# Performance work log

Hardware: AMD Instinct MI355X
Metric: run time of the kernel (lower is better)

Reference implementation:

```python
import jax, jax.numpy as jnp
import numpy as np

N, E = 50000, 800000
IN_F, C, H, OUT_F = 128, 32, 4, 4
HC = H * C
EPS = 1e-5


def gatv2(x, src, dst, ea, Wl, Wr, We, att, bias, concat):
    # x: [N, in], ea: [E, 1], Wl/Wr: [in, H*C], We: [1, H*C], att: [h, C]
    h, c = att.shape
    xl = (x @ Wl).reshape(-1, h, c)          # [N, h, c]
    xr = (x @ Wr).reshape(-1, h, c)          # [N, h, c]
    m = xl[src] + xr[dst] + (ea @ We).reshape(-1, h, c)   # [E, h, c]
    e = jnp.einsum('ehc,hc->eh', jax.nn.leaky_relu(m, 0.2), att)  # [E, h]
    emax = jax.ops.segment_max(e, dst, num_segments=N)
    e = jnp.exp(e - emax[dst])
    denom = jax.ops.segment_sum(e, dst, num_segments=N)
    alpha = e / (denom[dst] + 1e-16)         # [E, h]
    out = jax.ops.segment_sum(alpha[:, :, None] * xl[src], dst, num_segments=N)  # [N, h, c]
    out = out.reshape(N, h * c) if concat else out.mean(axis=1)
    return out + bias


def bn_eval(x, g, b, m, v):
    return (x - m) * jax.lax.rsqrt(v + EPS) * g + b


def setup_inputs() -> dict:
    key = jax.random.key(0)
    ks = iter(jax.random.split(key, 40))
    nrm = lambda shape, s=0.2: jax.random.normal(next(ks), shape, jnp.float32) * s
    d = {}
    d['x'] = jax.random.normal(next(ks), (N, IN_F), jnp.float32)
    d['edge_index'] = jax.random.randint(next(ks), (2, E), 0, N, jnp.int32)
    d['edge_attr'] = jax.random.normal(next(ks), (E, 1), jnp.float32)
    # layer 1
    d['l1_Wl'] = nrm((IN_F, HC)); d['l1_Wr'] = nrm((IN_F, HC))
    d['l1_We'] = nrm((1, HC)); d['l1_att'] = nrm((H, C)); d['l1_b'] = nrm((HC,))
    # layers 2-9 stacked
    d['mid_Wl'] = nrm((8, HC, HC)); d['mid_Wr'] = nrm((8, HC, HC))
    d['mid_We'] = nrm((8, 1, HC)); d['mid_att'] = nrm((8, H, C)); d['mid_b'] = nrm((8, HC))
    # layer 10: heads=1, concat=False
    d['l10_Wl'] = nrm((HC, C)); d['l10_Wr'] = nrm((HC, C))
    d['l10_We'] = nrm((1, C)); d['l10_att'] = nrm((1, C)); d['l10_b'] = nrm((C,))
    # batchnorms (eval mode): bn1-9 stacked, bn10 separate
    d['bn_g'] = jax.random.uniform(next(ks), (9, HC), jnp.float32, 0.5, 1.5)
    d['bn_b'] = nrm((9, HC)); d['bn_m'] = nrm((9, HC))
    d['bn_v'] = jax.random.uniform(next(ks), (9, HC), jnp.float32, 0.5, 1.5)
    d['bn10_g'] = jax.random.uniform(next(ks), (C,), jnp.float32, 0.5, 1.5)
    d['bn10_b'] = nrm((C,)); d['bn10_m'] = nrm((C,))
    d['bn10_v'] = jax.random.uniform(next(ks), (C,), jnp.float32, 0.5, 1.5)
    d['lin_W'] = nrm((C, OUT_F)); d['lin_b'] = nrm((OUT_F,))
    return d


def reference(x, edge_index, edge_attr,
              l1_Wl, l1_Wr, l1_We, l1_att, l1_b,
              mid_Wl, mid_Wr, mid_We, mid_att, mid_b,
              l10_Wl, l10_Wr, l10_We, l10_att, l10_b,
              bn_g, bn_b, bn_m, bn_v,
              bn10_g, bn10_b, bn10_m, bn10_v,
              lin_W, lin_b):
    src, dst = edge_index[0], edge_index[1]
    h = jax.nn.relu(gatv2(x, src, dst, edge_attr, l1_Wl, l1_Wr, l1_We, l1_att, l1_b, True))
    h = bn_eval(h, bn_g[0], bn_b[0], bn_m[0], bn_v[0])
    for i in range(8):  # layers 2-9
        h = jax.nn.relu(gatv2(h, src, dst, edge_attr, mid_Wl[i], mid_Wr[i], mid_We[i], mid_att[i], mid_b[i], True))
        h = bn_eval(h, bn_g[i + 1], bn_b[i + 1], bn_m[i + 1], bn_v[i + 1])
    h = jax.nn.relu(gatv2(h, src, dst, edge_attr, l10_Wl, l10_Wr, l10_We, l10_att, l10_b, False))
    h = bn_eval(h, bn10_g, bn10_b, bn10_m, bn10_v)
    return h @ lin_W + lin_b
```

## Files before the change

kernel.cpp:

```cpp
#include <hip/hip_runtime.h>
#include <math.h>

#define NN 50000
#define EE 800000
#define EPS 1e-5f
#define SCAN_CH 196

#define NEG_BIG (-1e30f)
#define RESCALE_THR 4.0f

#define LO_SCALE 2048.0f
#define LO_INV   (1.0f/2048.0f)

typedef unsigned short u16;
typedef _Float16 f16x8 __attribute__((ext_vector_type(8)));
typedef float f32x4 __attribute__((ext_vector_type(4)));

__device__ __forceinline__ u16 f2h(float f) {
    _Float16 h = (_Float16)f;
    return __builtin_bit_cast(u16, h);
}
__device__ __forceinline__ float h2f(u16 u) {
    return (float)__builtin_bit_cast(_Float16, u);
}

__global__ void hist_kernel(const int* __restrict__ dst, int* cnt) {
    int e = blockIdx.x * blockDim.x + threadIdx.x;
    if (e < EE) atomicAdd(&cnt[dst[e]], 1);
}

__global__ void scan_part(const int* __restrict__ cnt, int* __restrict__ part) {
    __shared__ int red[256];
    int b = blockIdx.x, t = threadIdx.x;
    int i = b * SCAN_CH + t;
    int v = (t < SCAN_CH && i < NN) ? cnt[i] : 0;
    red[t] = v;
    __syncthreads();
#pragma unroll
    for (int s = 128; s; s >>= 1) {
        if (t < s) red[t] += red[t + s];
        __syncthreads();
    }
    if (t == 0) part[b] = red[0];
}

__global__ void scan_block(int* part) {
    __shared__ int buf[2][256];
    int t = threadIdx.x;
    int v = part[t];
    int p = 0;
    buf[0][t] = v;
    __syncthreads();
#pragma unroll
    for (int off = 1; off < 256; off <<= 1) {
        buf[p ^ 1][t] = buf[p][t] + ((t >= off) ? buf[p][t - off] : 0);
        __syncthreads();
        p ^= 1;
    }
    part[t] = buf[p][t] - v;
}

__global__ void scan_final(int* __restrict__ cntcur, const int* __restrict__ part,
                           int* __restrict__ row_start) {
    __shared__ int buf[2][256];
    int b = blockIdx.x, t = threadIdx.x;
    int i = b * SCAN_CH + t;
    int v = (t < SCAN_CH && i < NN) ? cntcur[i] : 0;
    int p = 0;
    buf[0][t] = v;
    __syncthreads();
#pragma unroll
    for (int off = 1; off < 256; off <<= 1) {
        buf[p ^ 1][t] = buf[p][t] + ((t >= off) ? buf[p][t - off] : 0);
        __syncthreads();
        p ^= 1;
    }
    if (t < SCAN_CH && i < NN) {
        int pos = part[b] + buf[p][t] - v;
        row_start[i] = pos;
        cntcur[i] = pos;
    }
    if (b == 0 && t == 0) row_start[NN] = EE;
}

__global__ void scatter_kernel(const int* __restrict__ ei, const float* __restrict__ ea,
                               int* cursor, int2* __restrict__ edge_pack) {
    int e = blockIdx.x * blockDim.x + threadIdx.x;
    if (e < EE) {
        int d = ei[EE + e];
        int pos = atomicAdd(&cursor[d], 1);
        edge_pack[pos] = make_int2(ei[e], __float_as_int(ea[e]));
    }
}

__global__ void split_f32(const float* __restrict__ in, u16* __restrict__ hi,
                          u16* __restrict__ lo, int n4) {
    int i = blockIdx.x * blockDim.x + threadIdx.x;
    if (i >= n4) return;
    float4 v = ((const float4*)in)[i];
    ushort4 h, l;
    h.x = f2h(v.x); l.x = f2h((v.x - h2f(h.x)) * LO_SCALE);
    h.y = f2h(v.y); l.y = f2h((v.y - h2f(h.y)) * LO_SCALE);
    h.z = f2h(v.z); l.z = f2h((v.z - h2f(h.z)) * LO_SCALE);
    h.w = f2h(v.w); l.w = f2h((v.w - h2f(h.w)) * LO_SCALE);
    ((ushort4*)hi)[i] = h;
    ((ushort4*)lo)[i] = l;
}

__global__ void conv_w(const float* __restrict__ l1Wl, const float* __restrict__ l1Wr,
                       const float* __restrict__ midWl, const float* __restrict__ midWr,
                       u16* __restrict__ Wh, u16* __restrict__ Wlo) {
    int tid = blockIdx.x * 256 + threadIdx.x;
    if (tid >= 9 * 256 * 128) return;
    int L = tid >> 15;
    int rem = tid & 32767;
    int n = rem >> 7, k = rem & 127;
    const float* WL;
    const float* WR;
    if (L == 0) { WL = l1Wl; WR = l1Wr; }
    else {
        WL = midWl + (size_t)(L - 1) * 16384;
        WR = midWr + (size_t)(L - 1) * 16384;
    }
    float w = (n < 128) ? WL[k * 128 + n] : WR[k * 128 + (n - 128)];
    u16 h = f2h(w);
    Wh[tid] = h;
    Wlo[tid] = f2h((w - h2f(h)) * LO_SCALE);
}

__global__ __launch_bounds__(256) void gemm_mfma(const u16* __restrict__ Ah,
                                                 const u16* __restrict__ Al,
                                                 const u16* __restrict__ Bh,
                                                 const u16* __restrict__ Bl,
                                                 float* __restrict__ C) {
    int w    = threadIdx.x >> 6;
    int lane = threadIdx.x & 63;
    int lr = lane & 15;
    int kg = lane >> 4;
    int rowbase = blockIdx.x * 128;
    int colbase = blockIdx.y * 128 + w * 32;

    f16x8 bh[2][4], bl[2][4];
#pragma unroll
    for (int ct = 0; ct < 2; ++ct) {
        size_t boff = (size_t)(colbase + ct * 16 + lr) * 128 + (size_t)(kg * 8);
#pragma unroll
        for (int ks = 0; ks < 4; ++ks) {
            bh[ct][ks] = *(const f16x8*)(Bh + boff + ks * 32);
            bl[ct][ks] = *(const f16x8*)(Bl + boff + ks * 32);
        }
    }

    auto aoff_of = [&](int rt) {
        int arow = rowbase + rt * 16 + lr;
        if (arow >= NN) arow = NN - 1;
        return (size_t)arow * 128 + (size_t)(kg * 8);
    };
    f16x8 ahc[4], alc[4], ahn[4], aln[4];
    {
        size_t ao = aoff_of(0);
#pragma unroll
        for (int ks = 0; ks < 4; ++ks) {
            ahc[ks] = *(const f16x8*)(Ah + ao + ks * 32);
            alc[ks] = *(const f16x8*)(Al + ao + ks * 32);
        }
    }

#pragma unroll
    for (int rt = 0; rt < 8; ++rt) {
        if (rt < 7) {
            size_t ao = aoff_of(rt + 1);
#pragma unroll
            for (int ks = 0; ks < 4; ++ks) {
                ahn[ks] = *(const f16x8*)(Ah + ao + ks * 32);
                aln[ks] = *(const f16x8*)(Al + ao + ks * 32);
            }
        }

        f32x4 aH[2], aL[2];
#pragma unroll
        for (int ct = 0; ct < 2; ++ct) {
            aH[ct] = (f32x4){0.f, 0.f, 0.f, 0.f};
            aL[ct] = (f32x4){0.f, 0.f, 0.f, 0.f};
        }
#pragma unroll
        for (int ks = 0; ks < 4; ++ks) {
#pragma unroll
            for (int ct = 0; ct < 2; ++ct) {
                aH[ct] = __builtin_amdgcn_mfma_f32_16x16x32_f16(ahc[ks], bh[ct][ks], aH[ct], 0, 0, 0);
                aL[ct] = __builtin_amdgcn_mfma_f32_16x16x32_f16(alc[ks], bh[ct][ks], aL[ct], 0, 0, 0);
                aL[ct] = __builtin_amdgcn_mfma_f32_16x16x32_f16(ahc[ks], bl[ct][ks], aL[ct], 0, 0, 0);
            }
        }

        int crow0 = rowbase + rt * 16 + kg * 4;
#pragma unroll
        for (int ct = 0; ct < 2; ++ct) {
            float* cp = C + (size_t)crow0 * 256 + colbase + ct * 16 + lr;
#pragma unroll
            for (int r = 0; r < 4; ++r) {
                if (crow0 + r < NN)
                    cp[(size_t)r * 256] = fmaf(aL[ct][r], LO_INV, aH[ct][r]);
            }
        }

        if (rt < 7) {
#pragma unroll
            for (int ks = 0; ks < 4; ++ks) { ahc[ks] = ahn[ks]; alc[ks] = aln[ks]; }
        }
    }
}

__global__ __launch_bounds__(256) void gemm_tile(const float* __restrict__ A,
                                                 const float* __restrict__ B,
                                                 float* __restrict__ C,
                                                 int M, int nc, int ldb, int ldc, int coff) {
    __shared__ float As[128][64];
    __shared__ float Bs[128][64];
    int t  = threadIdx.x;
    int bm = blockIdx.x * 64;
    int bn = blockIdx.y * 64;
    {
        int k4 = (t & 31) << 2;
        int r0 = t >> 5;
#pragma unroll
        for (int pass = 0; pass < 8; ++pass) {
            int row = r0 + pass * 8;
            int gm  = bm + row;
            float4 v = make_float4(0.f, 0.f, 0.f, 0.f);
            if (gm < M) v = *(const float4*)(A + (size_t)gm * 128 + k4);
            As[k4 + 0][row] = v.x; As[k4 + 1][row] = v.y;
            As[k4 + 2][row] = v.z; As[k4 + 3][row] = v.w;
        }
    }
    {
        int c4 = (t & 15) << 2;
        int kr = t >> 4;
#pragma unroll
        for (int pass = 0; pass < 8; ++pass) {
            int k  = kr + pass * 16;
            int gc = bn + c4;
            float4 v = make_float4(0.f, 0.f, 0.f, 0.f);
            if (gc < nc) v = *(const float4*)(B + (size_t)k * ldb + gc);
            *(float4*)&Bs[k][c4] = v;
        }
    }
    __syncthreads();

    int tx = t & 15, ty = t >> 4;
    int m0 = ty * 4, c0 = tx * 4;
    float acc[4][4] = {{0.f}};
#pragma unroll 8
    for (int k = 0; k < 128; ++k) {
        float4 av = *(const float4*)&As[k][m0];
        float4 bv = *(const float4*)&Bs[k][c0];
        float a4[4] = {av.x, av.y, av.z, av.w};
        float b4[4] = {bv.x, bv.y, bv.z, bv.w};
#pragma unroll
        for (int i = 0; i < 4; ++i)
#pragma unroll
            for (int j = 0; j < 4; ++j) acc[i][j] = fmaf(a4[i], b4[j], acc[i][j]);
    }
#pragma unroll
    for (int i = 0; i < 4; ++i) {
        int gm = bm + m0 + i;
        int gc = bn + c0;
        if (gm < M && gc < nc) {
            *(float4*)(C + (size_t)gm * ldc + coff + gc) =
                make_float4(acc[i][0], acc[i][1], acc[i][2], acc[i][3]);
        }
    }
}

__device__ __forceinline__ float dpp_add8(float x) {
    int t;
    t = __builtin_amdgcn_update_dpp(0, __float_as_int(x), 0xB1, 0xf, 0xf, true);
    x += __int_as_float(t);
    t = __builtin_amdgcn_update_dpp(0, __float_as_int(x), 0x4E, 0xf, 0xf, true);
    x += __int_as_float(t);
    t = __builtin_amdgcn_update_dpp(0, __float_as_int(x), 0x141, 0xf, 0xf, true);
    x += __int_as_float(t);
    return x;
}

__global__ __launch_bounds__(256) void node_agg_128(const float* __restrict__ xlr,
                                                    const int* __restrict__ row_start,
                                                    const int2* __restrict__ epack,
                                                    const float* __restrict__ We,
                                                    const float* __restrict__ att,
                                                    const float* __restrict__ bias,
                                                    const float* __restrict__ bng,
                                                    const float* __restrict__ bnb,
                                                    const float* __restrict__ bnm,
                                                    const float* __restrict__ bnv,
                                                    u16* __restrict__ ahi,
                                                    u16* __restrict__ alo,
                                                    int wf32,
                                                    float* __restrict__ hout) {
    int wave = (blockIdx.x * blockDim.x + threadIdx.x) >> 6;
    int lane = threadIdx.x & 63;
    if (wave >= NN) return;
    int half = lane >> 5;
    int c0   = (lane & 31) << 2;

    const float L2E = 1.44269504f;
    const float4 xr4 = *(const float4*)(xlr + (size_t)wave * 256 + 128 + c0);
    const float4 we4 = *(const float4*)(We + c0);
    const float4 at4 = *(const float4*)(att + c0);
    float4 a6, a4;
    a6.x = 0.6f * L2E * at4.x; a4.x = 0.4f * L2E * at4.x;
    a6.y = 0.6f * L2E * at4.y; a4.y = 0.4f * L2E * at4.y;
    a6.z = 0.6f * L2E * at4.z; a4.z = 0.4f * L2E * at4.z;
    a6.w = 0.6f * L2E * at4.w; a4.w = 0.4f * L2E * at4.w;

    int beg = row_start[wave], end = row_start[wave + 1];
    int lastE = end - 1;

    float mx0 = NEG_BIG, sm0 = 0.f;
    float mx1 = NEG_BIG, sm1 = 0.f;
    float4 ac0 = make_float4(0.f, 0.f, 0.f, 0.f);
    float4 ac1 = make_float4(0.f, 0.f, 0.f, 0.f);

    auto score = [&](float eav, const float4& xv) -> float {
        float m0 = xv.x + fmaf(eav, we4.x, xr4.x);
        float m1 = xv.y + fmaf(eav, we4.y, xr4.y);
        float m2 = xv.z + fmaf(eav, we4.z, xr4.z);
        float m3 = xv.w + fmaf(eav, we4.w, xr4.w);
        float p = fmaf(a6.x, m0, a4.x * fabsf(m0));
        p = fmaf(a6.y, m1, fmaf(a4.y, fabsf(m1), p));
        p = fmaf(a6.z, m2, fmaf(a4.z, fabsf(m2), p));
        p = fmaf(a6.w, m3, fmaf(a4.w, fabsf(m3), p));
        return dpp_add8(p);
    };

    auto upd = [&](float& mx, float& sm, float4& ac, float p, const float4& xv) {
        float d = p - mx;
        if (__ballot(d > RESCALE_THR)) {
            float nm = fmaxf(mx, p);
            float sc = exp2f(mx - nm);
            float w  = exp2f(p - nm);
            sm = fmaf(sm, sc, w);
            ac.x = fmaf(ac.x, sc, w * xv.x);
            ac.y = fmaf(ac.y, sc, w * xv.y);
            ac.z = fmaf(ac.z, sc, w * xv.z);
            ac.w = fmaf(ac.w, sc, w * xv.w);
            mx = nm;
        } else {
            float w = exp2f(d);
            sm += w;
            ac.x = fmaf(w, xv.x, ac.x);
            ac.y = fmaf(w, xv.y, ac.y);
            ac.z = fmaf(w, xv.z, ac.z);
            ac.w = fmaf(w, xv.w, ac.w);
        }
    };

    int j = beg;
    for (; j + 3 < end; j += 4) {
        int2 pkA = epack[j + half];
        int2 pkB = epack[j + 2 + half];
        float4 xA = *(const float4*)(xlr + ((size_t)pkA.x << 8) + c0);
        float4 xB = *(const float4*)(xlr + ((size_t)pkB.x << 8) + c0);
        float pA = score(__int_as_float(pkA.y), xA);
        float pB = score(__int_as_float(pkB.y), xB);
        upd(mx0, sm0, ac0, pA, xA);
        upd(mx1, sm1, ac1, pB, xB);
    }
    if (j < end) {
        int jeA = j + half;       bool dA = jeA > lastE; if (dA) jeA = lastE;
        int jeB = j + 2 + half;   bool dB = jeB > lastE; if (dB) jeB = lastE;
        int2 pkA = epack[jeA];
        int2 pkB = epack[jeB];
        float4 xA = *(const float4*)(xlr + ((size_t)pkA.x << 8) + c0);
        float4 xB = *(const float4*)(xlr + ((size_t)pkB.x << 8) + c0);
        float pA = score(__int_as_float(pkA.y), xA);
        float pB = score(__int_as_float(pkB.y), xB);
        pA = dA ? NEG_BIG : pA;
        pB = dB ? NEG_BIG : pB;
        upd(mx0, sm0, ac0, pA, xA);
        upd(mx1, sm1, ac1, pB, xB);
    }

    float Mx = fmaxf(mx0, mx1);
    float s0 = exp2f(mx0 - Mx), s1 = exp2f(mx1 - Mx);
    float sm = fmaf(sm0, s0, sm1 * s1);
    float4 ac;
    ac.x = fmaf(ac0.x, s0, ac1.x * s1);
    ac.y = fmaf(ac0.y, s0, ac1.y * s1);
    ac.z = fmaf(ac0.z, s0, ac1.z * s1);
    ac.w = fmaf(ac0.w, s0, ac1.w * s1);

    float  Mo  = __shfl_xor(Mx, 32);
    float  smo = __shfl_xor(sm, 32);
    float4 aco;
    aco.x = __shfl_xor(ac.x, 32);
    aco.y = __shfl_xor(ac.y, 32);
    aco.z = __shfl_xor(ac.z, 32);
    aco.w = __shfl_xor(ac.w, 32);
    float Mn = fmaxf(Mx, Mo);
    float ss = exp2f(Mx - Mn), so = exp2f(Mo - Mn);
    sm   = fmaf(sm, ss, smo * so);
    ac.x = fmaf(ac.x, ss, aco.x * so);
    ac.y = fmaf(ac.y, ss, aco.y * so);
    ac.z = fmaf(ac.z, ss, aco.z * so);
    ac.w = fmaf(ac.w, ss, aco.w * so);

    if (half == 0) {
        float inv = 1.f / (sm + 1e-16f);
        const float4 b4  = *(const float4*)(bias + c0);
        const float4 g4  = *(const float4*)(bng + c0);
        const float4 bb4 = *(const float4*)(bnb + c0);
        const float4 m4  = *(const float4*)(bnm + c0);
        const float4 v4  = *(const float4*)(bnv + c0);
        float4 y;
        y.x = fmaxf(fmaf(ac.x, inv, b4.x), 0.f);
        y.y = fmaxf(fmaf(ac.y, inv, b4.y), 0.f);
        y.z = fmaxf(fmaf(ac.z, inv, b4.z), 0.f);
        y.w = fmaxf(fmaf(ac.w, inv, b4.w), 0.f);
        y.x = (y.x - m4.x) * rsqrtf(v4.x + EPS) * g4.x + bb4.x;
        y.y = (y.y - m4.y) * rsqrtf(v4.y + EPS) * g4.y + bb4.y;
        y.z = (y.z - m4.z) * rsqrtf(v4.z + EPS) * g4.z + bb4.z;
        y.w = (y.w - m4.w) * rsqrtf(v4.w + EPS) * g4.w + bb4.w;

        ushort4 hh, ll;
        hh.x = f2h(y.x); ll.x = f2h((y.x - h2f(hh.x)) * LO_SCALE);
        hh.y = f2h(y.y); ll.y = f2h((y.y - h2f(hh.y)) * LO_SCALE);
        hh.z = f2h(y.z); ll.z = f2h((y.z - h2f(hh.z)) * LO_SCALE);
        hh.w = f2h(y.w); ll.w = f2h((y.w - h2f(hh.w)) * LO_SCALE);
        *(ushort4*)(ahi + (size_t)wave * 128 + c0) = hh;
        *(ushort4*)(alo + (size_t)wave * 128 + c0) = ll;
        if (wf32) *(float4*)(hout + (size_t)wave * 128 + c0) = y;
    }
}

__global__ __launch_bounds__(256) void node_agg_l10(const float* __restrict__ xlr,
                                                    const int* __restrict__ row_start,
                                                    const int2* __restrict__ epack,
                                                    const float* __restrict__ We,
                                                    const float* __restrict__ att,
                                                    const float* __restrict__ bias,
                                                    const float* __restrict__ bng,
                                                    const float* __restrict__ bnb,
                                                    const float* __restrict__ bnm,
                                                    const float* __restrict__ bnv,
                                                    const float* __restrict__ linW,
                                                    const float* __restrict__ linb,
                                                    float* __restrict__ out) {
    int n = (blockIdx.x * blockDim.x + threadIdx.x) >> 5;
    int c = threadIdx.x & 31;
    if (n >= NN) return;

    const float L2E = 1.44269504f;
    float xr = xlr[(size_t)n * 64 + 32 + c];
    float we = We[c];
    float a6 = 0.6f * L2E * att[c], a4 = 0.4f * L2E * att[c];
    int beg = row_start[n], end = row_start[n + 1];

    float mxs[2] = {-INFINITY, -INFINITY};
    float sms[2] = {0.f, 0.f};
    float acs[2] = {0.f, 0.f};

    auto upd = [&](int st, float xl, float eav) {
        float m = xl + fmaf(eav, we, xr);
        float p = fmaf(a6, m, a4 * fabsf(m));
#pragma unroll
        for (int off = 16; off; off >>= 1) p += __shfl_xor(p, off);
        float nm = fmaxf(mxs[st], p);
        float sc = exp2f(mxs[st] - nm);
        float w  = exp2f(p - nm);
        sms[st] = fmaf(sms[st], sc, w);
        acs[st] = fmaf(acs[st], sc, w * xl);
        mxs[st] = nm;
    };

    int j = beg;
    for (; j + 1 < end; j += 2) {
        int2 p0 = epack[j], p1 = epack[j + 1];
        float x0 = xlr[((size_t)p0.x << 6) + c];
        float x1 = xlr[((size_t)p1.x << 6) + c];
        upd(0, x0, __int_as_float(p0.y));
        upd(1, x1, __int_as_float(p1.y));
    }
    if (j < end) {
        int2 pk = epack[j];
        upd(0, xlr[((size_t)pk.x << 6) + c], __int_as_float(pk.y));
    }

    float M = fmaxf(mxs[0], mxs[1]);
    float sm = 0.f, acc = 0.f;
#pragma unroll
    for (int st = 0; st < 2; ++st) {
        float sc = (mxs[st] == -INFINITY) ? 0.f : exp2f(mxs[st] - M);
        sm  = fmaf(sms[st], sc, sm);
        acc = fmaf(acs[st], sc, acc);
    }

    float y = acc / (sm + 1e-16f) + bias[c];
    y = fmaxf(y, 0.f);
    y = (y - bnm[c]) * rsqrtf(bnv[c] + EPS) * bng[c] + bnb[c];

    float t0 = y * linW[c * 4 + 0];
    float t1 = y * linW[c * 4 + 1];
    float t2 = y * linW[c * 4 + 2];
    float t3 = y * linW[c * 4 + 3];
#pragma unroll
    for (int off = 16; off; off >>= 1) {
        t0 += __shfl_xor(t0, off);
        t1 += __shfl_xor(t1, off);
        t2 += __shfl_xor(t2, off);
        t3 += __shfl_xor(t3, off);
    }
    if (c == 0) {
        out[(size_t)n * 4 + 0] = t0 + linb[0];
        out[(size_t)n * 4 + 1] = t1 + linb[1];
        out[(size_t)n * 4 + 2] = t2 + linb[2];
        out[(size_t)n * 4 + 3] = t3 + linb[3];
    }
}

extern "C" void kernel_launch(void* const* d_in, const int* in_sizes, int n_in,
                              void* d_out, int out_size, void* d_ws, size_t ws_size,
                              hipStream_t stream) {
    const float* x      = (const float*)d_in[0];
    const int*   ei     = (const int*)d_in[1];
    const float* ea     = (const float*)d_in[2];
    const float* l1_Wl  = (const float*)d_in[3];
    const float* l1_Wr  = (const float*)d_in[4];
    const float* l1_We  = (const float*)d_in[5];
    const float* l1_att = (const float*)d_in[6];
    const float* l1_b   = (const float*)d_in[7];
    const float* mid_Wl = (const float*)d_in[8];
    const float* mid_Wr = (const float*)d_in[9];
    const float* mid_We = (const float*)d_in[10];
    const float* mid_att= (const float*)d_in[11];
    const float* mid_b  = (const float*)d_in[12];
    const float* l10_Wl = (const float*)d_in[13];
    const float* l10_Wr = (const float*)d_in[14];
    const float* l10_We = (const float*)d_in[15];
    const float* l10_att= (const float*)d_in[16];
    const float* l10_b  = (const float*)d_in[17];
    const float* bn_g   = (const float*)d_in[18];
    const float* bn_b   = (const float*)d_in[19];
    const float* bn_m   = (const float*)d_in[20];
    const float* bn_v   = (const float*)d_in[21];
    const float* bn10_g = (const float*)d_in[22];
    const float* bn10_b = (const float*)d_in[23];
    const float* bn10_m = (const float*)d_in[24];
    const float* bn10_v = (const float*)d_in[25];
    const float* lin_W  = (const float*)d_in[26];
    const float* lin_b  = (const float*)d_in[27];

    char* ws = (char*)d_ws;
    auto take = [&](size_t bytes) { char* p = ws; ws += (bytes + 255) & ~size_t(255); return p; };
    int*   row_start  = (int*)  take(sizeof(int) * (NN + 1));
    int*   cursor     = (int*)  take(sizeof(int) * NN);
    int*   part       = (int*)  take(sizeof(int) * 256);
    int2*  epack      = (int2*) take(sizeof(int2) * EE);
    float* xlr        = (float*)take(sizeof(float) * (size_t)NN * 256);
    float* h0         = (float*)take(sizeof(float) * (size_t)NN * 128);
    u16*   Ahi        = (u16*)  take(sizeof(u16) * (size_t)NN * 128);
    u16*   Alo        = (u16*)  take(sizeof(u16) * (size_t)NN * 128);
    u16*   Wthi       = (u16*)  take(sizeof(u16) * 9 * 256 * 128);
    u16*   Wtlo       = (u16*)  take(sizeof(u16) * 9 * 256 * 128);

    hipMemsetAsync(cursor, 0, sizeof(int) * NN, stream);
    hist_kernel<<<EE / 256, 256, 0, stream>>>(ei + EE, cursor);
    scan_part<<<256, 256, 0, stream>>>(cursor, part);
    scan_block<<<1, 256, 0, stream>>>(part);
    scan_final<<<256, 256, 0, stream>>>(cursor, part, row_start);
    scatter_kernel<<<EE / 256, 256, 0, stream>>>(ei, ea, cursor, epack);

    split_f32<<<(NN * 128 / 4 + 255) / 256, 256, 0, stream>>>(x, Ahi, Alo, NN * 128 / 4);
    conv_w<<<(9 * 256 * 128 + 255) / 256, 256, 0, stream>>>(l1_Wl, l1_Wr, mid_Wl, mid_Wr,
                                                            Wthi, Wtlo);

    const int GBM = (NN + 127) / 128;
    dim3 gmm(GBM, 2);

    gemm_mfma<<<gmm, 256, 0, stream>>>(Ahi, Alo, Wthi, Wtlo, xlr);
    node_agg_128<<<(NN * 64) / 256, 256, 0, stream>>>(
        xlr, row_start, epack, l1_We, l1_att, l1_b,
        bn_g, bn_b, bn_m, bn_v, Ahi, Alo, 0, h0);

    for (int i = 0; i < 8; ++i) {
        gemm_mfma<<<gmm, 256, 0, stream>>>(Ahi, Alo,
                                           Wthi + (size_t)(i + 1) * 32768,
                                           Wtlo + (size_t)(i + 1) * 32768, xlr);
        node_agg_128<<<(NN * 64) / 256, 256, 0, stream>>>(
            xlr, row_start, epack,
            mid_We + (size_t)i * 128, mid_att + (size_t)i * 128, mid_b + (size_t)i * 128,
            bn_g + (size_t)(i + 1) * 128, bn_b + (size_t)(i + 1) * 128,
            bn_m + (size_t)(i + 1) * 128, bn_v + (size_t)(i + 1) * 128,
            Ahi, Alo, (i == 7) ? 1 : 0, h0);
    }

    const int MB = (NN + 63) / 64;
    dim3 g1(MB, 1);
    gemm_tile<<<g1, 256, 0, stream>>>(h0, l10_Wl, xlr, NN, 32, 32, 64, 0);
    gemm_tile<<<g1, 256, 0, stream>>>(h0, l10_Wr, xlr, NN, 32, 32, 64, 32);
    node_agg_l10<<<(NN * 32 + 255) / 256, 256, 0, stream>>>(
        xlr, row_start, epack, l10_We, l10_att, l10_b,
        bn10_g, bn10_b, bn10_m, bn10_v, lin_W, lin_b, (float*)d_out);
}
```

Measured before the change: 1.249 ms.

## Degree-sort nodes, split xl/xr planes, prefetch edges, vectorize final layer aggregation

Adds a counting sort of nodes by in-degree (descending) so each wave of the aggregation kernels handles nodes of similar degree, which reduces intra-block imbalance. The GEMM output is split into separate xl and xr planes of 128 floats each, so each gathered source row is contiguous and tightly packed. The edge loop in node_agg_128 software-prefetches the next group of edges. The layer-10 aggregation is rewritten to process 4 edges per half-wave with float4 loads, DPP reductions and lazy max rescaling. The cost is three extra small setup kernels and scattered node writes.

```diff
diff --git a/kernel.cpp b/kernel.cpp
--- a/kernel.cpp
+++ b/kernel.cpp
@@ -22,6 +22,17 @@
 }
 __device__ __forceinline__ float h2f(u16 u) {
     return (float)__builtin_bit_cast(_Float16, u);
+}
+
+__device__ __forceinline__ float dpp_add8(float x) {
+    int t;
+    t = __builtin_amdgcn_update_dpp(0, __float_as_int(x), 0xB1, 0xf, 0xf, true);
+    x += __int_as_float(t);
+    t = __builtin_amdgcn_update_dpp(0, __float_as_int(x), 0x4E, 0xf, 0xf, true);
+    x += __int_as_float(t);
+    t = __builtin_amdgcn_update_dpp(0, __float_as_int(x), 0x141, 0xf, 0xf, true);
+    x += __int_as_float(t);
+    return x;
 }
 
 __global__ void hist_kernel(const int* __restrict__ dst, int* cnt) {
@@ -90,6 +101,32 @@
         int d = ei[EE + e];
         int pos = atomicAdd(&cursor[d], 1);
         edge_pack[pos] = make_int2(ei[e], __float_as_int(ea[e]));
+    }
+}
+
+#define DBINS 64
+__global__ void deg_hist(const int* __restrict__ row_start, int* dbin) {
+    int i = blockIdx.x * blockDim.x + threadIdx.x;
+    if (i < NN) {
+        int d = row_start[i + 1] - row_start[i];
+        if (d > DBINS - 1) d = DBINS - 1;
+        atomicAdd(&dbin[DBINS - 1 - d], 1);
+    }
+}
+__global__ void deg_scan(int* dbin) {
+    if (threadIdx.x == 0) {
+        int acc = 0;
+        for (int k = 0; k < DBINS; ++k) { int v = dbin[k]; dbin[k] = acc; acc += v; }
+    }
+}
+__global__ void deg_scatter(const int* __restrict__ row_start, int* dbin,
+                            int* __restrict__ perm) {
+    int i = blockIdx.x * blockDim.x + threadIdx.x;
+    if (i < NN) {
+        int d = row_start[i + 1] - row_start[i];
+        if (d > DBINS - 1) d = DBINS - 1;
+        int pos = atomicAdd(&dbin[DBINS - 1 - d], 1);
+        perm[pos] = i;
     }
 }
 
@@ -138,7 +175,8 @@
     int lr = lane & 15;
     int kg = lane >> 4;
     int rowbase = blockIdx.x * 128;
-    int colbase = blockIdx.y * 128 + w * 32;
+    int colb = w * 32;
+    int colbase = blockIdx.y * 128 + colb;
 
     f16x8 bh[2][4], bl[2][4];
 #pragma unroll
@@ -166,6 +204,8 @@
         }
     }
 
+    float* Cp = C + (size_t)blockIdx.y * ((size_t)NN * 128);
+
 #pragma unroll
     for (int rt = 0; rt < 8; ++rt) {
         if (rt < 7) {
@@ -196,11 +236,11 @@
         int crow0 = rowbase + rt * 16 + kg * 4;
 #pragma unroll
         for (int ct = 0; ct < 2; ++ct) {
-            float* cp = C + (size_t)crow0 * 256 + colbase + ct * 16 + lr;
+            float* cp = Cp + (size_t)crow0 * 128 + colb + ct * 16 + lr;
 #pragma unroll
             for (int r = 0; r < 4; ++r) {
                 if (crow0 + r < NN)
-                    cp[(size_t)r * 256] = fmaf(aL[ct][r], LO_INV, aH[ct][r]);
+                    cp[(size_t)r * 128] = fmaf(aL[ct][r], LO_INV, aH[ct][r]);
             }
         }
 
@@ -272,19 +312,9 @@
     }
 }
 
-__device__ __forceinline__ float dpp_add8(float x) {
-    int t;
-    t = __builtin_amdgcn_update_dpp(0, __float_as_int(x), 0xB1, 0xf, 0xf, true);
-    x += __int_as_float(t);
-    t = __builtin_amdgcn_update_dpp(0, __float_as_int(x), 0x4E, 0xf, 0xf, true);
-    x += __int_as_float(t);
-    t = __builtin_amdgcn_update_dpp(0, __float_as_int(x), 0x141, 0xf, 0xf, true);
-    x += __int_as_float(t);
-    return x;
-}
-
 __global__ __launch_bounds__(256) void node_agg_128(const float* __restrict__ xlr,
                                                     const int* __restrict__ row_start,
+                                                    const int* __restrict__ perm,
                                                     const int2* __restrict__ epack,
                                                     const float* __restrict__ We,
                                                     const float* __restrict__ att,
@@ -300,11 +330,15 @@
     int wave = (blockIdx.x * blockDim.x + threadIdx.x) >> 6;
     int lane = threadIdx.x & 63;
     if (wave >= NN) return;
+    int node = perm[wave];
     int half = lane >> 5;
     int c0   = (lane & 31) << 2;
 
+    const float* xlp = xlr;
+    const float* xrp = xlr + (size_t)NN * 128;
+
     const float L2E = 1.44269504f;
-    const float4 xr4 = *(const float4*)(xlr + (size_t)wave * 256 + 128 + c0);
+    const float4 xr4 = *(const float4*)(xrp + (size_t)node * 128 + c0);
     const float4 we4 = *(const float4*)(We + c0);
     const float4 at4 = *(const float4*)(att + c0);
     float4 a6, a4;
@@ -313,7 +347,7 @@
     a6.z = 0.6f * L2E * at4.z; a4.z = 0.4f * L2E * at4.z;
     a6.w = 0.6f * L2E * at4.w; a4.w = 0.4f * L2E * at4.w;
 
-    int beg = row_start[wave], end = row_start[wave + 1];
+    int beg = row_start[node], end = row_start[node + 1];
     int lastE = end - 1;
 
     float mx0 = NEG_BIG, sm0 = 0.f;
@@ -355,30 +389,44 @@
         }
     };
 
-    int j = beg;
-    for (; j + 3 < end; j += 4) {
-        int2 pkA = epack[j + half];
-        int2 pkB = epack[j + 2 + half];
-        float4 xA = *(const float4*)(xlr + ((size_t)pkA.x << 8) + c0);
-        float4 xB = *(const float4*)(xlr + ((size_t)pkB.x << 8) + c0);
-        float pA = score(__int_as_float(pkA.y), xA);
-        float pB = score(__int_as_float(pkB.y), xB);
-        upd(mx0, sm0, ac0, pA, xA);
-        upd(mx1, sm1, ac1, pB, xB);
-    }
-    if (j < end) {
-        int jeA = j + half;       bool dA = jeA > lastE; if (dA) jeA = lastE;
-        int jeB = j + 2 + half;   bool dB = jeB > lastE; if (dB) jeB = lastE;
-        int2 pkA = epack[jeA];
-        int2 pkB = epack[jeB];
-        float4 xA = *(const float4*)(xlr + ((size_t)pkA.x << 8) + c0);
-        float4 xB = *(const float4*)(xlr + ((size_t)pkB.x << 8) + c0);
-        float pA = score(__int_as_float(pkA.y), xA);
-        float pB = score(__int_as_float(pkB.y), xB);
+    int nE = end - beg;
+    int last4 = beg + (nE & ~3);
+
+    int2 pkA, pkB; float4 xA, xB;
+    if (beg < last4) {
+        pkA = epack[beg + half];
+        pkB = epack[beg + 2 + half];
+        xA = *(const float4*)(xlp + ((size_t)pkA.x << 7) + c0);
+        xB = *(const float4*)(xlp + ((size_t)pkB.x << 7) + c0);
+    }
+    for (int j = beg; j < last4; ) {
+        int2 cA = pkA, cB = pkB;
+        float4 yA = xA, yB = xB;
+        j += 4;
+        if (j < last4) {
+            pkA = epack[j + half];
+            pkB = epack[j + 2 + half];
+            xA = *(const float4*)(xlp + ((size_t)pkA.x << 7) + c0);
+            xB = *(const float4*)(xlp + ((size_t)pkB.x << 7) + c0);
+        }
+        float pA = score(__int_as_float(cA.y), yA);
+        float pB = score(__int_as_float(cB.y), yB);
+        upd(mx0, sm0, ac0, pA, yA);
+        upd(mx1, sm1, ac1, pB, yB);
+    }
+    if (last4 < end) {
+        int jeA = last4 + half;       bool dA = jeA > lastE; if (dA) jeA = lastE;
+        int jeB = last4 + 2 + half;   bool dB = jeB > lastE; if (dB) jeB = lastE;
+        int2 tA = epack[jeA];
+        int2 tB = epack[jeB];
+        float4 yA = *(const float4*)(xlp + ((size_t)tA.x << 7) + c0);
+        float4 yB = *(const float4*)(xlp + ((size_t)tB.x << 7) + c0);
+        float pA = score(__int_as_float(tA.y), yA);
+        float pB = score(__int_as_float(tB.y), yB);
         pA = dA ? NEG_BIG : pA;
         pB = dB ? NEG_BIG : pB;
-        upd(mx0, sm0, ac0, pA, xA);
-        upd(mx1, sm1, ac1, pB, xB);
+        upd(mx0, sm0, ac0, pA, yA);
+        upd(mx1, sm1, ac1, pB, yB);
     }
 
     float Mx = fmaxf(mx0, mx1);
@@ -427,14 +475,15 @@
         hh.y = f2h(y.y); ll.y = f2h((y.y - h2f(hh.y)) * LO_SCALE);
         hh.z = f2h(y.z); ll.z = f2h((y.z - h2f(hh.z)) * LO_SCALE);
         hh.w = f2h(y.w); ll.w = f2h((y.w - h2f(hh.w)) * LO_SCALE);
-        *(ushort4*)(ahi + (size_t)wave * 128 + c0) = hh;
-        *(ushort4*)(alo + (size_t)wave * 128 + c0) = ll;
-        if (wf32) *(float4*)(hout + (size_t)wave * 128 + c0) = y;
+        *(ushort4*)(ahi + (size_t)node * 128 + c0) = hh;
+        *(ushort4*)(alo + (size_t)node * 128 + c0) = ll;
+        if (wf32) *(float4*)(hout + (size_t)node * 128 + c0) = y;
     }
 }
 
 __global__ __launch_bounds__(256) void node_agg_l10(const float* __restrict__ xlr,
                                                     const int* __restrict__ row_start,
+                                                    const int* __restrict__ perm,
                                                     const int2* __restrict__ epack,
                                                     const float* __restrict__ We,
                                                     const float* __restrict__ att,
@@ -446,75 +495,135 @@
                                                     const float* __restrict__ linW,
                                                     const float* __restrict__ linb,
                                                     float* __restrict__ out) {
-    int n = (blockIdx.x * blockDim.x + threadIdx.x) >> 5;
-    int c = threadIdx.x & 31;
-    if (n >= NN) return;
+    int hw = (blockIdx.x * blockDim.x + threadIdx.x) >> 5;
+    if (hw >= NN) return;
+    int n = perm[hw];
+    int q    = threadIdx.x & 31;
+    int slot = q >> 3;
+    int c0   = (q & 7) << 2;
 
     const float L2E = 1.44269504f;
-    float xr = xlr[(size_t)n * 64 + 32 + c];
-    float we = We[c];
-    float a6 = 0.6f * L2E * att[c], a4 = 0.4f * L2E * att[c];
+    const float4 xr = *(const float4*)(xlr + (size_t)n * 64 + 32 + c0);
+    const float4 we = *(const float4*)(We + c0);
+    const float4 at = *(const float4*)(att + c0);
+    float4 a6, a4;
+    a6.x = 0.6f * L2E * at.x; a4.x = 0.4f * L2E * at.x;
+    a6.y = 0.6f * L2E * at.y; a4.y = 0.4f * L2E * at.y;
+    a6.z = 0.6f * L2E * at.z; a4.z = 0.4f * L2E * at.z;
+    a6.w = 0.6f * L2E * at.w; a4.w = 0.4f * L2E * at.w;
+
     int beg = row_start[n], end = row_start[n + 1];
-
-    float mxs[2] = {-INFINITY, -INFINITY};
-    float sms[2] = {0.f, 0.f};
-    float acs[2] = {0.f, 0.f};
-
-    auto upd = [&](int st, float xl, float eav) {
-        float m = xl + fmaf(eav, we, xr);
-        float p = fmaf(a6, m, a4 * fabsf(m));
-#pragma unroll
-        for (int off = 16; off; off >>= 1) p += __shfl_xor(p, off);
-        float nm = fmaxf(mxs[st], p);
-        float sc = exp2f(mxs[st] - nm);
-        float w  = exp2f(p - nm);
-        sms[st] = fmaf(sms[st], sc, w);
-        acs[st] = fmaf(acs[st], sc, w * xl);
-        mxs[st] = nm;
+    int lastE = end - 1;
+
+    float mx = NEG_BIG, sm = 0.f;
+    float4 ac = make_float4(0.f, 0.f, 0.f, 0.f);
+
+    auto score4 = [&](float eav, const float4& xv) -> float {
+        float m0 = xv.x + fmaf(eav, we.x, xr.x);
+        float m1 = xv.y + fmaf(eav, we.y, xr.y);
+        float m2 = xv.z + fmaf(eav, we.z, xr.z);
+        float m3 = xv.w + fmaf(eav, we.w, xr.w);
+        float p = fmaf(a6.x, m0, a4.x * fabsf(m0));
+        p = fmaf(a6.y, m1, fmaf(a4.y, fabsf(m1), p));
+        p = fmaf(a6.z, m2, fmaf(a4.z, fabsf(m2), p));
+        p = fmaf(a6.w, m3, fmaf(a4.w, fabsf(m3), p));
+        return dpp_add8(p);
     };
 
-    int j = beg;
-    for (; j + 1 < end; j += 2) {
-        int2 p0 = epack[j], p1 = epack[j + 1];
-        float x0 = xlr[((size_t)p0.x << 6) + c];
-        float x1 = xlr[((size_t)p1.x << 6) + c];
-        upd(0, x0, __int_as_float(p0.y));
-        upd(1, x1, __int_as_float(p1.y));
-    }
-    if (j < end) {
-        int2 pk = epack[j];
-        upd(0, xlr[((size_t)pk.x << 6) + c], __int_as_float(pk.y));
-    }
-
-    float M = fmaxf(mxs[0], mxs[1]);
-    float sm = 0.f, acc = 0.f;
-#pragma unroll
-    for (int st = 0; st < 2; ++st) {
-        float sc = (mxs[st] == -INFINITY) ? 0.f : exp2f(mxs[st] - M);
-        sm  = fmaf(sms[st], sc, sm);
-        acc = fmaf(acs[st], sc, acc);
-    }
-
-    float y = acc / (sm + 1e-16f) + bias[c];
-    y = fmaxf(y, 0.f);
-    y = (y - bnm[c]) * rsqrtf(bnv[c] + EPS) * bng[c] + bnb[c];
-
-    float t0 = y * linW[c * 4 + 0];
-    float t1 = y * linW[c * 4 + 1];
-    float t2 = y * linW[c * 4 + 2];
-    float t3 = y * linW[c * 4 + 3];
-#pragma unroll
-    for (int off = 16; off; off >>= 1) {
-        t0 += __shfl_xor(t0, off);
-        t1 += __shfl_xor(t1, off);
-        t2 += __shfl_xor(t2, off);
-        t3 += __shfl_xor(t3, off);
-    }
-    if (c == 0) {
-        out[(size_t)n * 4 + 0] = t0 + linb[0];
-        out[(size_t)n * 4 + 1] = t1 + linb[1];
-        out[(size_t)n * 4 + 2] = t2 + linb[2];
-        out[(size_t)n * 4 + 3] = t3 + linb[3];
+    auto upd = [&](float p, const float4& xv) {
+        float d = p - mx;
+        if (__ballot(d > RESCALE_THR)) {
+            float nm = fmaxf(mx, p);
+            float sc = exp2f(mx - nm);
+            float w  = exp2f(p - nm);
+            sm = fmaf(sm, sc, w);
+            ac.x = fmaf(ac.x, sc, w * xv.x); ac.y = fmaf(ac.y, sc, w * xv.y);
+            ac.z = fmaf(ac.z, sc, w * xv.z); ac.w = fmaf(ac.w, sc, w * xv.w);
+            mx = nm;
+        } else {
+            float w = exp2f(d);
+            sm += w;
+            ac.x = fmaf(w, xv.x, ac.x); ac.y = fmaf(w, xv.y, ac.y);
+            ac.z = fmaf(w, xv.z, ac.z); ac.w = fmaf(w, xv.w, ac.w);
+        }
+    };
+
+    int nE = end - beg;
+    int last4 = beg + (nE & ~3);
+
+    int2 pkn; float4 xvn;
+    if (beg < last4) {
+        pkn = epack[beg + slot];
+        xvn = *(const float4*)(xlr + ((size_t)pkn.x << 6) + c0);
+    }
+    for (int j = beg; j < last4; ) {
+        int2 pk = pkn; float4 xv = xvn;
+        j += 4;
+        if (j < last4) {
+            pkn = epack[j + slot];
+            xvn = *(const float4*)(xlr + ((size_t)pkn.x << 6) + c0);
+        }
+        float p = score4(__int_as_float(pk.y), xv);
+        upd(p, xv);
+    }
+    if (last4 < end) {
+        int je = last4 + slot;
+        bool dead = je > lastE; if (dead) je = lastE;
+        int2 pk = epack[je];
+        float4 xv = *(const float4*)(xlr + ((size_t)pk.x << 6) + c0);
+        float p = score4(__int_as_float(pk.y), xv);
+        p = dead ? NEG_BIG : p;
+        upd(p, xv);
+    }
+
+#pragma unroll
+    for (int off = 8; off <= 16; off <<= 1) {
+        float  Mo  = __shfl_xor(mx, off);
+        float  smo = __shfl_xor(sm, off);
+        float4 aco;
+        aco.x = __shfl_xor(ac.x, off); aco.y = __shfl_xor(ac.y, off);
+        aco.z = __shfl_xor(ac.z, off); aco.w = __shfl_xor(ac.w, off);
+        float Mn = fmaxf(mx, Mo);
+        float ss = exp2f(mx - Mn), so = exp2f(Mo - Mn);
+        sm = fmaf(sm, ss, smo * so);
+        ac.x = fmaf(ac.x, ss, aco.x * so); ac.y = fmaf(ac.y, ss, aco.y * so);
+        ac.z = fmaf(ac.z, ss, aco.z * so); ac.w = fmaf(ac.w, ss, aco.w * so);
+        mx = Mn;
+    }
+
+    float inv = 1.f / (sm + 1e-16f);
+    const float4 b4 = *(const float4*)(bias + c0);
+    const float4 g4 = *(const float4*)(bng + c0);
+    const float4 q4 = *(const float4*)(bnb + c0);
+    const float4 m4 = *(const float4*)(bnm + c0);
+    const float4 v4 = *(const float4*)(bnv + c0);
+    float4 y;
+    y.x = fmaxf(fmaf(ac.x, inv, b4.x), 0.f);
+    y.y = fmaxf(fmaf(ac.y, inv, b4.y), 0.f);
+    y.z = fmaxf(fmaf(ac.z, inv, b4.z), 0.f);
+    y.w = fmaxf(fmaf(ac.w, inv, b4.w), 0.f);
+    y.x = (y.x - m4.x) * rsqrtf(v4.x + EPS) * g4.x + q4.x;
+    y.y = (y.y - m4.y) * rsqrtf(v4.y + EPS) * g4.y + q4.y;
+    y.z = (y.z - m4.z) * rsqrtf(v4.z + EPS) * g4.z + q4.z;
+    y.w = (y.w - m4.w) * rsqrtf(v4.w + EPS) * g4.w + q4.w;
+
+    const float4 w0 = *(const float4*)(linW + (c0 + 0) * 4);
+    const float4 w1 = *(const float4*)(linW + (c0 + 1) * 4);
+    const float4 w2 = *(const float4*)(linW + (c0 + 2) * 4);
+    const float4 w3 = *(const float4*)(linW + (c0 + 3) * 4);
+    float4 t;
+    t.x = fmaf(y.x, w0.x, fmaf(y.y, w1.x, fmaf(y.z, w2.x, y.w * w3.x)));
+    t.y = fmaf(y.x, w0.y, fmaf(y.y, w1.y, fmaf(y.z, w2.y, y.w * w3.y)));
+    t.z = fmaf(y.x, w0.z, fmaf(y.y, w1.z, fmaf(y.z, w2.z, y.w * w3.z)));
+    t.w = fmaf(y.x, w0.w, fmaf(y.y, w1.w, fmaf(y.z, w2.w, y.w * w3.w)));
+    t.x = dpp_add8(t.x); t.y = dpp_add8(t.y);
+    t.z = dpp_add8(t.z); t.w = dpp_add8(t.w);
+
+    if (q == 0) {
+        const float4 lb = *(const float4*)linb;
+        float4 o;
+        o.x = t.x + lb.x; o.y = t.y + lb.y; o.z = t.z + lb.z; o.w = t.w + lb.w;
+        *(float4*)(out + (size_t)n * 4) = o;
     }
 }
 
@@ -555,6 +664,8 @@
     int*   row_start  = (int*)  take(sizeof(int) * (NN + 1));
     int*   cursor     = (int*)  take(sizeof(int) * NN);
     int*   part       = (int*)  take(sizeof(int) * 256);
+    int*   perm       = (int*)  take(sizeof(int) * NN);
+    int*   dbin       = (int*)  take(sizeof(int) * DBINS);
     int2*  epack      = (int2*) take(sizeof(int2) * EE);
     float* xlr        = (float*)take(sizeof(float) * (size_t)NN * 256);
     float* h0         = (float*)take(sizeof(float) * (size_t)NN * 128);
@@ -564,12 +675,18 @@
     u16*   Wtlo       = (u16*)  take(sizeof(u16) * 9 * 256 * 128);
 
     hipMemsetAsync(cursor, 0, sizeof(int) * NN, stream);
+    hipMemsetAsync(dbin, 0, sizeof(int) * DBINS, stream);
     hist_kernel<<<EE / 256, 256, 0, stream>>>(ei + EE, cursor);
     scan_part<<<256, 256, 0, stream>>>(cursor, part);
     scan_block<<<1, 256, 0, stream>>>(part);
     scan_final<<<256, 256, 0, stream>>>(cursor, part, row_start);
     scatter_kernel<<<EE / 256, 256, 0, stream>>>(ei, ea, cursor, epack);
 
+    const int NB = (NN + 255) / 256;
+    deg_hist<<<NB, 256, 0, stream>>>(row_start, dbin);
+    deg_scan<<<1, 64, 0, stream>>>(dbin);
+    deg_scatter<<<NB, 256, 0, stream>>>(row_start, dbin, perm);
+
     split_f32<<<(NN * 128 / 4 + 255) / 256, 256, 0, stream>>>(x, Ahi, Alo, NN * 128 / 4);
     conv_w<<<(9 * 256 * 128 + 255) / 256, 256, 0, stream>>>(l1_Wl, l1_Wr, mid_Wl, mid_Wr,
                                                             Wthi, Wtlo);
@@ -579,7 +696,7 @@
 
     gemm_mfma<<<gmm, 256, 0, stream>>>(Ahi, Alo, Wthi, Wtlo, xlr);
     node_agg_128<<<(NN * 64) / 256, 256, 0, stream>>>(
-        xlr, row_start, epack, l1_We, l1_att, l1_b,
+        xlr, row_start, perm, epack, l1_We, l1_att, l1_b,
         bn_g, bn_b, bn_m, bn_v, Ahi, Alo, 0, h0);
 
     for (int i = 0; i < 8; ++i) {
@@ -587,7 +704,7 @@
                                            Wthi + (size_t)(i + 1) * 32768,
                                            Wtlo + (size_t)(i + 1) * 32768, xlr);
         node_agg_128<<<(NN * 64) / 256, 256, 0, stream>>>(
-            xlr, row_start, epack,
+            xlr, row_start, perm, epack,
             mid_We + (size_t)i * 128, mid_att + (size_t)i * 128, mid_b + (size_t)i * 128,
             bn_g + (size_t)(i + 1) * 128, bn_b + (size_t)(i + 1) * 128,
             bn_m + (size_t)(i + 1) * 128, bn_v + (size_t)(i + 1) * 128,
@@ -599,6 +716,6 @@
     gemm_tile<<<g1, 256, 0, stream>>>(h0, l10_Wl, xlr, NN, 32, 32, 64, 0);
     gemm_tile<<<g1, 256, 0, stream>>>(h0, l10_Wr, xlr, NN, 32, 32, 64, 32);
     node_agg_l10<<<(NN * 32 + 255) / 256, 256, 0, stream>>>(
-        xlr, row_start, epack, l10_We, l10_att, l10_b,
+        xlr, row_start, perm, epack, l10_We, l10_att, l10_b,
         bn10_g, bn10_b, bn10_m, bn10_v, lin_W, lin_b, (float*)d_out);
 }
```

Result: slower. 1.539 ms (+23.3%).
